# Kernel optimization log

Hardware: AMD Instinct MI355X
Metric: run time of the kernel (lower is better)

Reference implementation:

```python
import math
import jax, jax.numpy as jnp
import numpy as np

S = 2048   # padded sequence length (both src and tgt)
B = 8      # batch
D = 512    # d_embed
K = 64     # num_neighbors


def setup_inputs() -> dict:
    key = jax.random.key(0)
    ks = jax.random.split(key, 12)
    f32 = jnp.float32
    src_feats = jax.random.normal(ks[0], (S, B, D), f32)
    tgt_feats = jax.random.normal(ks[1], (S, B, D), f32)
    src_xyz = jax.random.normal(ks[2], (S, B, 3), f32)
    tgt_xyz = jax.random.normal(ks[3], (S, B, 3), f32)
    # lengths in [S - S//8, S] so every row has plenty of valid keys (>= K)
    src_lens = S - jax.random.randint(ks[4], (B,), 0, S // 8)
    tgt_lens = S - jax.random.randint(ks[5], (B,), 0, S // 8)
    scale = 1.0 / math.sqrt(D)
    Wq = jax.random.normal(ks[6], (D, D), f32) * scale
    bq = jnp.zeros((D,), f32)
    Wk = jax.random.normal(ks[7], (D, D), f32) * scale
    bk = jnp.zeros((D,), f32)
    Wc = jax.random.normal(ks[8], (1, D), f32) * scale
    bc = jnp.zeros((1,), f32)
    return dict(src_feats_padded=src_feats, tgt_feats_padded=tgt_feats,
                src_xyz_padded=src_xyz, tgt_xyz_padded=tgt_xyz,
                src_lens=src_lens, tgt_lens=tgt_lens,
                Wq=Wq, bq=bq, Wk=Wk, bk=bk, Wc=Wc, bc=bc)


def _simple_attention(query, key, value, key_padding_mask, Wq, bq, Wk, bk, num_neighbors):
    # query: (Q,B,D), key: (S,B,D), value: (S,B,E), key_padding_mask: (B,S) True=pad
    d = query.shape[-1]
    q = (query @ Wq.T + bq) / math.sqrt(d)          # (Q,B,D)
    k = key @ Wk.T + bk                              # (S,B,D)
    attn = jnp.einsum('qbd,sbd->bqs', q, k)          # (B,Q,S)
    attn = attn + jnp.where(key_padding_mask, -jnp.inf, 0.0)[:, None, :]
    if num_neighbors > 0:
        # Faithful to torch's `neighbor_mask[:, :, haha] = 0` (advanced indexing):
        # the UNION of top-k column indices over all (b,q) rows is unmasked for
        # every row; all other columns get -inf.
        idx = jax.lax.top_k(attn, num_neighbors)[1]              # (B,Q,K)
        col_mask = jnp.full((attn.shape[-1],), -jnp.inf, attn.dtype)
        col_mask = col_mask.at[idx.reshape(-1)].set(0.0)         # (S,)
        attn = attn + col_mask[None, None, :]
    attn = jax.nn.softmax(attn, axis=-1)
    return jnp.einsum('bqs,sbe->qbe', attn, value)   # (Q,B,E)


def _forward(src_feats, tgt_feats, src_xyz, tgt_xyz, src_lens, tgt_lens,
             Wq, bq, Wk, bk, Wc, bc):
    n_src, b = src_feats.shape[0], src_feats.shape[1]
    n_tgt = tgt_feats.shape[0]
    src_kpm = jnp.arange(n_src)[None, :] >= src_lens[:, None]   # (B,N_src)
    tgt_kpm = jnp.arange(n_tgt)[None, :] >= tgt_lens[:, None]   # (B,N_tgt)
    src_corr = _simple_attention(src_feats, tgt_feats, tgt_xyz, tgt_kpm,
                                 Wq, bq, Wk, bk, K)             # (N_src,B,3)
    tgt_corr = _simple_attention(tgt_feats, src_feats, src_xyz, src_kpm,
                                 Wq, bq, Wk, bk, K)             # (N_tgt,B,3)
    src_overlap = src_feats @ Wc.T + bc                          # (N_src,B,1)
    tgt_overlap = tgt_feats @ Wc.T + bc                          # (N_tgt,B,1)
    return src_corr, tgt_corr, src_overlap, tgt_overlap


def reference(src_feats_padded, tgt_feats_padded, src_xyz_padded, tgt_xyz_padded,
              src_lens, tgt_lens, Wq, bq, Wk, bk, Wc, bc):
    return _forward(src_feats_padded, tgt_feats_padded, src_xyz_padded,
                    tgt_xyz_padded, src_lens, tgt_lens, Wq, bq, Wk, bk, Wc, bc)
```

## Files before the change

### kernel.cpp

```cpp
#include <hip/hip_runtime.h>

typedef __attribute__((ext_vector_type(8))) short short8;
typedef __attribute__((ext_vector_type(4))) float f32x4;

#define SEQ 2048
#define BAT 8
#define DIM 512
#define RSQRT_D 0.044194173824159216f

__device__ __forceinline__ unsigned short f2bf(float x) {
  union { float f; unsigned u; } v; v.f = x;
  unsigned r = (v.u + 0x7FFFu + ((v.u >> 16) & 1u)) >> 16;
  return (unsigned short)r;
}

__device__ __forceinline__ unsigned char f2fp8(float x) {
  return (unsigned char)(__builtin_amdgcn_cvt_pk_fp8_f32(x, x, 0, false) & 0xFF);
}

__device__ __forceinline__ void gload_lds16(const void* g, void* lds_base) {
  __builtin_amdgcn_global_load_lds(
      (const __attribute__((address_space(1))) unsigned int*)g,
      (__attribute__((address_space(3))) unsigned int*)lds_base,
      16, 0, 0);
}

__global__ __launch_bounds__(256) void k_pack_feats(
    const float* __restrict__ src, const float* __restrict__ tgt,
    const float* __restrict__ Wc, const float* __restrict__ bc,
    unsigned short* __restrict__ srcT, unsigned short* __restrict__ tgtT,
    float* __restrict__ out) {
  int w = threadIdx.x >> 6, lane = threadIdx.x & 63;
  int row = blockIdx.x * 4 + w;
  int which = blockIdx.y;
  const float* in = (which ? tgt : src) + (size_t)row * DIM;
  unsigned short* T = which ? tgtT : srcT;
  int s = row >> 3, b = row & 7;

  const float4* in4 = (const float4*)in;
  float4 f0 = in4[lane * 2], f1 = in4[lane * 2 + 1];

  uint4 pk;
  pk.x = (unsigned)f2bf(f0.x) | ((unsigned)f2bf(f0.y) << 16);
  pk.y = (unsigned)f2bf(f0.z) | ((unsigned)f2bf(f0.w) << 16);
  pk.z = (unsigned)f2bf(f1.x) | ((unsigned)f2bf(f1.y) << 16);
  pk.w = (unsigned)f2bf(f1.z) | ((unsigned)f2bf(f1.w) << 16);
  *(uint4*)(T + ((size_t)(b * SEQ + s) * DIM + lane * 8)) = pk;

  const float4* wc4 = (const float4*)Wc;
  float4 w0 = wc4[lane * 2], w1 = wc4[lane * 2 + 1];
  float d = f0.x * w0.x + f0.y * w0.y + f0.z * w0.z + f0.w * w0.w +
            f1.x * w1.x + f1.y * w1.y + f1.z * w1.z + f1.w * w1.w;
  for (int o = 32; o; o >>= 1) d += __shfl_xor(d, o);
  if (lane == 0) {
    int base = which ? (SEQ * BAT * 6 + SEQ * BAT) : (SEQ * BAT * 6);
    out[base + row] = d + bc[0];
  }
}

__global__ __launch_bounds__(256) void k_misc_pack(
    const float* __restrict__ sxyz, const float* __restrict__ txyz,
    const float* __restrict__ Wq, const float* __restrict__ Wk,
    float4* __restrict__ Vsrc, float4* __restrict__ Vtgt,
    unsigned short* __restrict__ Wqb, unsigned short* __restrict__ Wkb) {
  int t = blockIdx.x * 256 + threadIdx.x;
  if (t < 32768) {
    int which = t >> 14, id = t & 16383;
    int s = id >> 3, b = id & 7;
    const float* xyz = (which ? txyz : sxyz) + (size_t)id * 3;
    float4 v = make_float4(xyz[0], xyz[1], xyz[2], 0.f);
    (which ? Vtgt : Vsrc)[b * SEQ + s] = v;
  } else {
    int i = t - 32768;
    int which = i >> 15, j = i & 32767;
    const float* wp = (which ? Wk : Wq) + (size_t)j * 8;
    unsigned short* o = which ? Wkb : Wqb;
    float4 f0 = *(const float4*)wp, f1 = *(const float4*)(wp + 4);
    uint4 pk;
    pk.x = (unsigned)f2bf(f0.x) | ((unsigned)f2bf(f0.y) << 16);
    pk.y = (unsigned)f2bf(f0.z) | ((unsigned)f2bf(f0.w) << 16);
    pk.z = (unsigned)f2bf(f1.x) | ((unsigned)f2bf(f1.y) << 16);
    pk.w = (unsigned)f2bf(f1.z) | ((unsigned)f2bf(f1.w) << 16);
    *(uint4*)(o + (size_t)j * 8) = pk;
  }
}

__global__ __launch_bounds__(256) void k_proj(
    const unsigned short* __restrict__ srcT, const unsigned short* __restrict__ tgtT,
    const unsigned short* __restrict__ Wqb, const unsigned short* __restrict__ Wkb,
    const float* __restrict__ bq, const float* __restrict__ bk,
    unsigned char* __restrict__ Qsrc, unsigned char* __restrict__ Ktgt,
    unsigned char* __restrict__ Qtgt, unsigned char* __restrict__ Ksrc) {
  __shared__ __align__(16) char at[16384];
  __shared__ __align__(16) char bt[16384];
  int z = blockIdx.z;
  bool isQ = (z == 0 || z == 2);
  const unsigned short* A = (z == 0 || z == 3) ? srcT : tgtT;
  const unsigned short* W = isQ ? Wqb : Wkb;
  const float* bias = isQ ? bq : bk;
  unsigned char* O = z == 0 ? Qsrc : z == 1 ? Ktgt : z == 2 ? Qtgt : Ksrc;

  int m0 = blockIdx.x * 128, n0 = blockIdx.y * 128;
  int tid = threadIdx.x, w = tid >> 6, lane = tid & 63;
  int ln = lane & 15, quad = lane >> 4;
  int moff = (w & 1) * 64, noff = (w >> 1) * 64;

  f32x4 acc[4][4];
  f32x4 zero = {0.f, 0.f, 0.f, 0.f};
  for (int mi = 0; mi < 4; ++mi)
    for (int ni = 0; ni < 4; ++ni) acc[mi][ni] = zero;

  for (int kb = 0; kb < DIM; kb += 64) {
    #pragma unroll
    for (int it = 0; it < 4; ++it) {
      int rbase = w * 32 + it * 8;
      int n = rbase + (lane >> 3);
      int c = (lane & 7) ^ (n & 7);
      gload_lds16(A + ((size_t)(m0 + n) * DIM + kb + c * 8), &at[rbase * 128]);
      gload_lds16(W + ((size_t)(n0 + n) * DIM + kb + c * 8), &bt[rbase * 128]);
    }
    __syncthreads();
    #pragma unroll
    for (int ks = 0; ks < 2; ++ks) {
      short8 afr[4], bfr[4];
      #pragma unroll
      for (int mi = 0; mi < 4; ++mi) {
        int r = moff + mi * 16 + ln;
        int p = (ks * 4 + quad) ^ (r & 7);
        afr[mi] = *(const short8*)(&at[r * 128 + p * 16]);
      }
      #pragma unroll
      for (int ni = 0; ni < 4; ++ni) {
        int r = noff + ni * 16 + ln;
        int p = (ks * 4 + quad) ^ (r & 7);
        bfr[ni] = *(const short8*)(&bt[r * 128 + p * 16]);
      }
      #pragma unroll
      for (int mi = 0; mi < 4; ++mi)
        #pragma unroll
        for (int ni = 0; ni < 4; ++ni)
          acc[mi][ni] = __builtin_amdgcn_mfma_f32_16x16x32_bf16(afr[mi], bfr[ni], acc[mi][ni], 0, 0, 0);
    }
    __syncthreads();
  }

  for (int ni = 0; ni < 4; ++ni) {
    int n_g = n0 + noff + ni * 16 + ln;
    float bv = bias[n_g];
    for (int mi = 0; mi < 4; ++mi) {
      int m_g = m0 + moff + mi * 16 + quad * 4;
      for (int r = 0; r < 4; ++r) {
        float v = acc[mi][ni][r] + bv;
        int row = m_g + r;
        size_t pos;
        if (isQ) pos = (size_t)row * DIM + n_g;
        else     pos = (size_t)row * DIM + ((((n_g >> 3) ^ (row & 15)) << 3) | (n_g & 7));
        O[pos] = f2fp8(v);
      }
    }
  }
}

__global__ __launch_bounds__(256) void k_attn(
    const unsigned char* __restrict__ Qsrc, const unsigned char* __restrict__ Ktgt,
    const unsigned char* __restrict__ Qtgt, const unsigned char* __restrict__ Ksrc,
    const float4* __restrict__ Vsrc, const float4* __restrict__ Vtgt,
    const int* __restrict__ src_lens, const int* __restrict__ tgt_lens,
    float4* __restrict__ part) {
  __shared__ __align__(16) char klds[32768];
  __shared__ float vx[512], vy[512], vz[512];
  int id = blockIdx.x;
  int x = id & 7, j = id >> 3;
  int group = (j >> 7) * 8 + x;
  int dir = group >> 3, b = group & 7;
  int inner = j & 127;
  int chunk = inner >> 5, qb = inner & 31;

  const unsigned char* Q = dir ? Qtgt : Qsrc;
  const unsigned char* K = dir ? Ksrc : Ktgt;
  const float4* V = dir ? Vsrc : Vtgt;
  int len = (dir ? src_lens : tgt_lens)[b];
  int k0g = chunk * 512;
  int kend = min(len, k0g + 512);
  int nblk = (kend - k0g + 31) >> 5;

  int tid = threadIdx.x, w = tid >> 6, lane = tid & 63;
  int ln = lane & 15, quad = lane >> 4;
  int q0 = qb * 64 + w * 16;

  for (int i = tid; i < 512; i += 256) {
    float4 vv = V[b * SEQ + k0g + i];
    vx[i] = vv.x; vy[i] = vv.y; vz[i] = vv.z;
  }

  long af[16];
  {
    const unsigned char* qrow = Q + (size_t)(b * SEQ + q0 + ln) * DIM + quad * 8;
    #pragma unroll
    for (int kk = 0; kk < 16; ++kk)
      af[kk] = *(const long*)(qrow + kk * 32);
  }

  float l_r[4], Ox[4], Oy[4], Oz[4];
  #pragma unroll
  for (int r = 0; r < 4; ++r) { l_r[r] = 0.f; Ox[r] = Oy[r] = Oz[r] = 0.f; }

  const unsigned char* kchunk = K + (size_t)(b * SEQ + k0g) * DIM;

  auto stage = [&](int kb, int bs) {
    const unsigned char* kbase = kchunk + (size_t)kb * 32 * DIM;
    char* dst = &klds[bs * 16384];
    #pragma unroll
    for (int it = 0; it < 4; ++it) {
      int rp = w * 4 + it;
      gload_lds16(kbase + rp * 1024 + lane * 16, dst + rp * 1024);
    }
  };

  stage(0, 0);
  __syncthreads();

  for (int kb = 0; kb < nblk; ++kb) {
    int bs = kb & 1;
    if (kb + 1 < nblk) stage(kb + 1, bs ^ 1);
    const char* buf = &klds[bs * 16384];
    const char* krow0 = buf + ln * DIM;
    const char* krow1 = buf + (16 + ln) * DIM;

    f32x4 acc0 = {0.f, 0.f, 0.f, 0.f}, acc1 = {0.f, 0.f, 0.f, 0.f};
    #pragma unroll
    for (int kk = 0; kk < 16; ++kk) {
      int pos = (((kk * 4 + quad) ^ ln) << 3);
      long b0 = *(const long*)(krow0 + pos);
      long b1 = *(const long*)(krow1 + pos);
      acc0 = __builtin_amdgcn_mfma_f32_16x16x32_fp8_fp8(af[kk], b0, acc0, 0, 0, 0);
      acc1 = __builtin_amdgcn_mfma_f32_16x16x32_fp8_fp8(af[kk], b1, acc1, 0, 0, 0);
    }

    int lk0 = kb * 32 + ln, lk1 = lk0 + 16;
    bool v0 = (k0g + lk0) < kend, v1 = (k0g + lk1) < kend;
    float Vx0 = vx[lk0], Vy0 = vy[lk0], Vz0 = vz[lk0];
    float Vx1 = vx[lk1], Vy1 = vy[lk1], Vz1 = vz[lk1];
    #pragma unroll
    for (int r = 0; r < 4; ++r) {
      float p0 = v0 ? __expf(acc0[r] * RSQRT_D) : 0.f;
      float p1 = v1 ? __expf(acc1[r] * RSQRT_D) : 0.f;
      l_r[r] += p0 + p1;
      Ox[r] += p0 * Vx0 + p1 * Vx1;
      Oy[r] += p0 * Vy0 + p1 * Vy1;
      Oz[r] += p0 * Vz0 + p1 * Vz1;
    }
    __syncthreads();
  }

  #pragma unroll
  for (int r = 0; r < 4; ++r) {
    float v0 = l_r[r], v1 = Ox[r], v2 = Oy[r], v3 = Oz[r];
    #pragma unroll
    for (int o = 1; o < 16; o <<= 1) {
      v0 += __shfl_xor(v0, o);
      v1 += __shfl_xor(v1, o);
      v2 += __shfl_xor(v2, o);
      v3 += __shfl_xor(v3, o);
    }
    if (ln == 0) {
      int q = q0 + quad * 4 + r;
      part[((size_t)(dir * BAT + b) * 4 + chunk) * SEQ + q] =
          make_float4(v0, v1, v2, v3);
    }
  }
}

__global__ __launch_bounds__(256) void k_attn_reduce(
    const float4* __restrict__ part, float* __restrict__ out) {
  int t = blockIdx.x * 256 + threadIdx.x;
  int dir = t >> 14, rem = t & 16383, b = rem >> 11, q = rem & 2047;
  size_t base = ((size_t)(dir * BAT + b) * 4) * SEQ + q;
  float4 s0 = part[base];
  float4 s1 = part[base + SEQ];
  float4 s2 = part[base + 2 * SEQ];
  float4 s3 = part[base + 3 * SEQ];
  float inv = 1.f / (s0.x + s1.x + s2.x + s3.x);
  float* ob = out + (size_t)dir * (SEQ * BAT * 3) + ((size_t)q * BAT + b) * 3;
  ob[0] = (s0.y + s1.y + s2.y + s3.y) * inv;
  ob[1] = (s0.z + s1.z + s2.z + s3.z) * inv;
  ob[2] = (s0.w + s1.w + s2.w + s3.w) * inv;
}

extern "C" void kernel_launch(void* const* d_in, const int* in_sizes, int n_in,
                              void* d_out, int out_size, void* d_ws, size_t ws_size,
                              hipStream_t stream) {
  const float* src  = (const float*)d_in[0];
  const float* tgt  = (const float*)d_in[1];
  const float* sxyz = (const float*)d_in[2];
  const float* txyz = (const float*)d_in[3];
  const int* slens  = (const int*)d_in[4];
  const int* tlens  = (const int*)d_in[5];
  const float* Wq   = (const float*)d_in[6];
  const float* bq   = (const float*)d_in[7];
  const float* Wk   = (const float*)d_in[8];
  const float* bk   = (const float*)d_in[9];
  const float* Wc   = (const float*)d_in[10];
  const float* bc   = (const float*)d_in[11];
  float* out = (float*)d_out;

  char* ws = (char*)d_ws;
  size_t off = 0;
  auto carve = [&](size_t bytes) -> char* {
    char* p = ws + off;
    off += (bytes + 255) & ~(size_t)255;
    return p;
  };
  const size_t FEAT_BF  = (size_t)BAT * SEQ * DIM * 2;
  const size_t FEAT_FP8 = (size_t)BAT * SEQ * DIM;
  unsigned short* srcT = (unsigned short*)carve(FEAT_BF);
  unsigned short* tgtT = (unsigned short*)carve(FEAT_BF);
  unsigned char* Qsrc = (unsigned char*)carve(FEAT_FP8);
  unsigned char* Ktgt = (unsigned char*)carve(FEAT_FP8);
  unsigned char* Qtgt = (unsigned char*)carve(FEAT_FP8);
  unsigned char* Ksrc = (unsigned char*)carve(FEAT_FP8);
  unsigned short* Wqb  = (unsigned short*)carve((size_t)DIM * DIM * 2);
  unsigned short* Wkb  = (unsigned short*)carve((size_t)DIM * DIM * 2);
  float4* Vsrc = (float4*)carve((size_t)BAT * SEQ * 16);
  float4* Vtgt = (float4*)carve((size_t)BAT * SEQ * 16);
  float4* part = (float4*)srcT;

  k_pack_feats<<<dim3(4096, 2), 256, 0, stream>>>(src, tgt, Wc, bc, srcT, tgtT, out);
  k_misc_pack<<<dim3(384), 256, 0, stream>>>(sxyz, txyz, Wq, Wk, Vsrc, Vtgt, Wqb, Wkb);
  k_proj<<<dim3(128, 4, 4), 256, 0, stream>>>(srcT, tgtT, Wqb, Wkb, bq, bk,
                                              Qsrc, Ktgt, Qtgt, Ksrc);
  k_attn<<<dim3(2048), 256, 0, stream>>>(Qsrc, Ktgt, Qtgt, Ksrc, Vsrc, Vtgt,
                                         slens, tlens, part);
  k_attn_reduce<<<dim3(128), 256, 0, stream>>>(part, out);
}
```

Baseline: 253.4 us.

## Merge pack kernels, remap proj grid, stream V from global in attention

Folds the small xyz/weight packing kernel into the feature packing kernel, which removes one launch. Flattens the projection grid into a 1-D index with an XCD-aware mapping so neighbouring blocks share A rows. In the attention kernel, V is loaded per block straight from global memory instead of being staged in shared memory, and the accumulation is split into a mask-free main path and a masked tail path that use packed float2 math. These changes trade extra global V loads and more code against less LDS use, fewer launches and cheaper inner-loop arithmetic.

```diff
diff --git a/kernel.cpp b/kernel.cpp
--- a/kernel.cpp
+++ b/kernel.cpp
@@ -2,6 +2,7 @@
 
 typedef __attribute__((ext_vector_type(8))) short short8;
 typedef __attribute__((ext_vector_type(4))) float f32x4;
+typedef __attribute__((ext_vector_type(2))) float f32x2;
 
 #define SEQ 2048
 #define BAT 8
@@ -25,14 +26,40 @@
       16, 0, 0);
 }
 
-__global__ __launch_bounds__(256) void k_pack_feats(
+__global__ __launch_bounds__(256) void k_pack(
     const float* __restrict__ src, const float* __restrict__ tgt,
     const float* __restrict__ Wc, const float* __restrict__ bc,
+    const float* __restrict__ sxyz, const float* __restrict__ txyz,
+    const float* __restrict__ Wq, const float* __restrict__ Wk,
     unsigned short* __restrict__ srcT, unsigned short* __restrict__ tgtT,
+    float4* __restrict__ Vsrc, float4* __restrict__ Vtgt,
+    unsigned short* __restrict__ Wqb, unsigned short* __restrict__ Wkb,
     float* __restrict__ out) {
+  int which = blockIdx.y;
+  if (blockIdx.x >= 4096) {
+    int e = (blockIdx.x - 4096) * 256 + threadIdx.x;
+    if (which == 0) {
+      int wsel = e >> 15, j = e & 32767;
+      const float* wp = (wsel ? Wk : Wq) + (size_t)j * 8;
+      unsigned short* o = wsel ? Wkb : Wqb;
+      float4 f0 = *(const float4*)wp, f1 = *(const float4*)(wp + 4);
+      uint4 pk;
+      pk.x = (unsigned)f2bf(f0.x) | ((unsigned)f2bf(f0.y) << 16);
+      pk.y = (unsigned)f2bf(f0.z) | ((unsigned)f2bf(f0.w) << 16);
+      pk.z = (unsigned)f2bf(f1.x) | ((unsigned)f2bf(f1.y) << 16);
+      pk.w = (unsigned)f2bf(f1.z) | ((unsigned)f2bf(f1.w) << 16);
+      *(uint4*)(o + (size_t)j * 8) = pk;
+    } else if (e < 32768) {
+      int wsel = e >> 14, id = e & 16383;
+      int s = id >> 3, b = id & 7;
+      const float* xyz = (wsel ? txyz : sxyz) + (size_t)id * 3;
+      float4 v = make_float4(xyz[0], xyz[1], xyz[2], 0.f);
+      (wsel ? Vtgt : Vsrc)[b * SEQ + s] = v;
+    }
+    return;
+  }
   int w = threadIdx.x >> 6, lane = threadIdx.x & 63;
   int row = blockIdx.x * 4 + w;
-  int which = blockIdx.y;
   const float* in = (which ? tgt : src) + (size_t)row * DIM;
   unsigned short* T = which ? tgtT : srcT;
   int s = row >> 3, b = row & 7;
@@ -58,33 +85,6 @@
   }
 }
 
-__global__ __launch_bounds__(256) void k_misc_pack(
-    const float* __restrict__ sxyz, const float* __restrict__ txyz,
-    const float* __restrict__ Wq, const float* __restrict__ Wk,
-    float4* __restrict__ Vsrc, float4* __restrict__ Vtgt,
-    unsigned short* __restrict__ Wqb, unsigned short* __restrict__ Wkb) {
-  int t = blockIdx.x * 256 + threadIdx.x;
-  if (t < 32768) {
-    int which = t >> 14, id = t & 16383;
-    int s = id >> 3, b = id & 7;
-    const float* xyz = (which ? txyz : sxyz) + (size_t)id * 3;
-    float4 v = make_float4(xyz[0], xyz[1], xyz[2], 0.f);
-    (which ? Vtgt : Vsrc)[b * SEQ + s] = v;
-  } else {
-    int i = t - 32768;
-    int which = i >> 15, j = i & 32767;
-    const float* wp = (which ? Wk : Wq) + (size_t)j * 8;
-    unsigned short* o = which ? Wkb : Wqb;
-    float4 f0 = *(const float4*)wp, f1 = *(const float4*)(wp + 4);
-    uint4 pk;
-    pk.x = (unsigned)f2bf(f0.x) | ((unsigned)f2bf(f0.y) << 16);
-    pk.y = (unsigned)f2bf(f0.z) | ((unsigned)f2bf(f0.w) << 16);
-    pk.z = (unsigned)f2bf(f1.x) | ((unsigned)f2bf(f1.y) << 16);
-    pk.w = (unsigned)f2bf(f1.z) | ((unsigned)f2bf(f1.w) << 16);
-    *(uint4*)(o + (size_t)j * 8) = pk;
-  }
-}
-
 __global__ __launch_bounds__(256) void k_proj(
     const unsigned short* __restrict__ srcT, const unsigned short* __restrict__ tgtT,
     const unsigned short* __restrict__ Wqb, const unsigned short* __restrict__ Wkb,
@@ -93,14 +93,18 @@
     unsigned char* __restrict__ Qtgt, unsigned char* __restrict__ Ksrc) {
   __shared__ __align__(16) char at[16384];
   __shared__ __align__(16) char bt[16384];
-  int z = blockIdx.z;
+  int id = blockIdx.x;
+  int x = id & 7, t = id >> 3;
+  int m = x * 16 + (t >> 4);
+  int inner = t & 15;
+  int n = inner & 3, z = inner >> 2;
   bool isQ = (z == 0 || z == 2);
   const unsigned short* A = (z == 0 || z == 3) ? srcT : tgtT;
   const unsigned short* W = isQ ? Wqb : Wkb;
   const float* bias = isQ ? bq : bk;
   unsigned char* O = z == 0 ? Qsrc : z == 1 ? Ktgt : z == 2 ? Qtgt : Ksrc;
 
-  int m0 = blockIdx.x * 128, n0 = blockIdx.y * 128;
+  int m0 = m * 128, n0 = n * 128;
   int tid = threadIdx.x, w = tid >> 6, lane = tid & 63;
   int ln = lane & 15, quad = lane >> 4;
   int moff = (w & 1) * 64, noff = (w >> 1) * 64;
@@ -114,10 +118,10 @@
     #pragma unroll
     for (int it = 0; it < 4; ++it) {
       int rbase = w * 32 + it * 8;
-      int n = rbase + (lane >> 3);
-      int c = (lane & 7) ^ (n & 7);
-      gload_lds16(A + ((size_t)(m0 + n) * DIM + kb + c * 8), &at[rbase * 128]);
-      gload_lds16(W + ((size_t)(n0 + n) * DIM + kb + c * 8), &bt[rbase * 128]);
+      int r = rbase + (lane >> 3);
+      int c = (lane & 7) ^ (r & 7);
+      gload_lds16(A + ((size_t)(m0 + r) * DIM + kb + c * 8), &at[rbase * 128]);
+      gload_lds16(W + ((size_t)(n0 + r) * DIM + kb + c * 8), &bt[rbase * 128]);
     }
     __syncthreads();
     #pragma unroll
@@ -168,7 +172,6 @@
     const int* __restrict__ src_lens, const int* __restrict__ tgt_lens,
     float4* __restrict__ part) {
   __shared__ __align__(16) char klds[32768];
-  __shared__ float vx[512], vy[512], vz[512];
   int id = blockIdx.x;
   int x = id & 7, j = id >> 3;
   int group = (j >> 7) * 8 + x;
@@ -182,17 +185,14 @@
   int len = (dir ? src_lens : tgt_lens)[b];
   int k0g = chunk * 512;
   int kend = min(len, k0g + 512);
-  int nblk = (kend - k0g + 31) >> 5;
+  int nk = kend - k0g;
+  int nblk = (nk + 31) >> 5;
+  bool tail = (nk & 31) != 0;
 
   int tid = threadIdx.x, w = tid >> 6, lane = tid & 63;
   int ln = lane & 15, quad = lane >> 4;
   int q0 = qb * 64 + w * 16;
 
-  for (int i = tid; i < 512; i += 256) {
-    float4 vv = V[b * SEQ + k0g + i];
-    vx[i] = vv.x; vy[i] = vv.y; vz[i] = vv.z;
-  }
-
   long af[16];
   {
     const unsigned char* qrow = Q + (size_t)(b * SEQ + q0 + ln) * DIM + quad * 8;
@@ -201,9 +201,10 @@
       af[kk] = *(const long*)(qrow + kk * 32);
   }
 
-  float l_r[4], Ox[4], Oy[4], Oz[4];
+  f32x2 l2[4], Ox2[4], Oy2[4], Oz2[4];
+  f32x2 z2 = {0.f, 0.f};
   #pragma unroll
-  for (int r = 0; r < 4; ++r) { l_r[r] = 0.f; Ox[r] = Oy[r] = Oz[r] = 0.f; }
+  for (int r = 0; r < 4; ++r) { l2[r] = z2; Ox2[r] = z2; Oy2[r] = z2; Oz2[r] = z2; }
 
   const unsigned char* kchunk = K + (size_t)(b * SEQ + k0g) * DIM;
 
@@ -238,24 +239,38 @@
     }
 
     int lk0 = kb * 32 + ln, lk1 = lk0 + 16;
-    bool v0 = (k0g + lk0) < kend, v1 = (k0g + lk1) < kend;
-    float Vx0 = vx[lk0], Vy0 = vy[lk0], Vz0 = vz[lk0];
-    float Vx1 = vx[lk1], Vy1 = vy[lk1], Vz1 = vz[lk1];
-    #pragma unroll
-    for (int r = 0; r < 4; ++r) {
-      float p0 = v0 ? __expf(acc0[r] * RSQRT_D) : 0.f;
-      float p1 = v1 ? __expf(acc1[r] * RSQRT_D) : 0.f;
-      l_r[r] += p0 + p1;
-      Ox[r] += p0 * Vx0 + p1 * Vx1;
-      Oy[r] += p0 * Vy0 + p1 * Vy1;
-      Oz[r] += p0 * Vz0 + p1 * Vz1;
+    float4 V0 = V[b * SEQ + k0g + lk0];
+    float4 V1 = V[b * SEQ + k0g + lk1];
+    f32x2 vxx = {V0.x, V1.x}, vyy = {V0.y, V1.y}, vzz = {V0.z, V1.z};
+    if (kb + 1 < nblk || !tail) {
+      #pragma unroll
+      for (int r = 0; r < 4; ++r) {
+        f32x2 p2;
+        p2.x = __expf(acc0[r] * RSQRT_D);
+        p2.y = __expf(acc1[r] * RSQRT_D);
+        l2[r] += p2;
+        Ox2[r] += p2 * vxx; Oy2[r] += p2 * vyy; Oz2[r] += p2 * vzz;
+      }
+    } else {
+      bool v0 = lk0 < nk, v1 = lk1 < nk;
+      #pragma unroll
+      for (int r = 0; r < 4; ++r) {
+        f32x2 p2;
+        p2.x = v0 ? __expf(acc0[r] * RSQRT_D) : 0.f;
+        p2.y = v1 ? __expf(acc1[r] * RSQRT_D) : 0.f;
+        l2[r] += p2;
+        Ox2[r] += p2 * vxx; Oy2[r] += p2 * vyy; Oz2[r] += p2 * vzz;
+      }
     }
     __syncthreads();
   }
 
   #pragma unroll
   for (int r = 0; r < 4; ++r) {
-    float v0 = l_r[r], v1 = Ox[r], v2 = Oy[r], v3 = Oz[r];
+    float v0 = l2[r].x + l2[r].y;
+    float v1 = Ox2[r].x + Ox2[r].y;
+    float v2 = Oy2[r].x + Oy2[r].y;
+    float v3 = Oz2[r].x + Oz2[r].y;
     #pragma unroll
     for (int o = 1; o < 16; o <<= 1) {
       v0 += __shfl_xor(v0, o);
@@ -325,10 +340,10 @@
   float4* Vtgt = (float4*)carve((size_t)BAT * SEQ * 16);
   float4* part = (float4*)srcT;
 
-  k_pack_feats<<<dim3(4096, 2), 256, 0, stream>>>(src, tgt, Wc, bc, srcT, tgtT, out);
-  k_misc_pack<<<dim3(384), 256, 0, stream>>>(sxyz, txyz, Wq, Wk, Vsrc, Vtgt, Wqb, Wkb);
-  k_proj<<<dim3(128, 4, 4), 256, 0, stream>>>(srcT, tgtT, Wqb, Wkb, bq, bk,
-                                              Qsrc, Ktgt, Qtgt, Ksrc);
+  k_pack<<<dim3(4352, 2), 256, 0, stream>>>(src, tgt, Wc, bc, sxyz, txyz, Wq, Wk,
+                                            srcT, tgtT, Vsrc, Vtgt, Wqb, Wkb, out);
+  k_proj<<<dim3(2048), 256, 0, stream>>>(srcT, tgtT, Wqb, Wkb, bq, bk,
+                                         Qsrc, Ktgt, Qtgt, Ksrc);
   k_attn<<<dim3(2048), 256, 0, stream>>>(Qsrc, Ktgt, Qtgt, Ksrc, Vsrc, Vtgt,
                                          slens, tlens, part);
   k_attn_reduce<<<dim3(128), 256, 0, stream>>>(part, out);
```

Result: slower. 265.4 us (+4.7%).
